# Performance work log

Hardware: AMD Instinct MI355X
Metric: run time of the kernel (lower is better)

Reference implementation:

```python
import jax, jax.numpy as jnp
import numpy as np


def setup_inputs() -> dict:
    key = jax.random.key(0)
    ks = jax.random.split(key, 4)
    B, S, D, U = 4, 4096, 128, 64
    x = jax.random.normal(ks[0], (B, S, D), dtype=jnp.float32)
    Wq = jax.random.normal(ks[1], (D, U), dtype=jnp.float32) * (1.0 / np.sqrt(D))
    Wk = jax.random.normal(ks[2], (D, U), dtype=jnp.float32) * (1.0 / np.sqrt(D))
    Wv = jax.random.normal(ks[3], (D, U), dtype=jnp.float32) * (1.0 / np.sqrt(D))
    bq = jnp.zeros((U,), dtype=jnp.float32)
    bk = jnp.zeros((U,), dtype=jnp.float32)
    bv = jnp.zeros((U,), dtype=jnp.float32)
    return {"x": x, "Wq": Wq, "bq": bq, "Wk": Wk, "bk": bk, "Wv": Wv, "bv": bv}


def reference(x, Wq, bq, Wk, bk, Wv, bv):
    # Single-head, unscaled, unmasked attention (faithful to the Keras layer).
    q = jnp.einsum("bsd,du->bsu", x, Wq) + bq  # [B,S,U]
    k = jnp.einsum("bsd,du->bsu", x, Wk) + bk  # [B,S,U]
    v = jnp.einsum("bsd,du->bsu", x, Wv) + bv  # [B,S,U]
    scores = jnp.einsum("bsu,btu->bst", q, k)  # [B,S,S], no 1/sqrt(d) scaling
    attn = jax.nn.softmax(scores, axis=-1)
    return jnp.einsum("bst,btu->bsu", attn, v)  # [B,S,U]
```

## Files before the change

### kernel.cpp

```cpp
#include <hip/hip_runtime.h>
#include <hip/hip_fp16.h>
#include <math.h>

#define SEQ   4096
#define DIM   128
#define UDIM  64
#define BATCH 4
#define BS    (BATCH*SEQ)
#define NT    (SEQ/64)
#define NSPLIT 6

typedef _Float16 h8 __attribute__((ext_vector_type(8)));
typedef _Float16 h4 __attribute__((ext_vector_type(4)));
typedef _Float16 h2 __attribute__((ext_vector_type(2)));
typedef float    f4 __attribute__((ext_vector_type(4)));

#define MFMA_K32(a,b,c) __builtin_amdgcn_mfma_f32_16x16x32_f16((a),(b),(c),0,0,0)

__device__ __forceinline__ h2 pk2(float a, float b) {
  return __builtin_bit_cast(h2, __builtin_amdgcn_cvt_pkrtz(a, b));
}
__device__ __forceinline__ float fexp2(float x) {
#if __has_builtin(__builtin_amdgcn_exp2f)
  return __builtin_amdgcn_exp2f(x);
#else
  return exp2f(x);
#endif
}

#define WT_STRIDE 272
#define KB_STRIDE 144
#define L2E 1.44269504088896f


__global__ __launch_bounds__(256, 2) void proj_mfma(
    const float* __restrict__ x,
    const float* __restrict__ Wq, const float* __restrict__ bq,
    const float* __restrict__ Wk, const float* __restrict__ bk,
    const float* __restrict__ Wv, const float* __restrict__ bv,
    _Float16* __restrict__ qf, _Float16* __restrict__ kswz, _Float16* __restrict__ vswz)
{
  const int tid  = threadIdx.x;
  const int lane = tid & 63, wv = tid >> 6;
  const int n = lane & 15, quad = lane >> 4;
  const int r0 = blockIdx.x * 64;

  __shared__ __align__(16) char wlds[3][UDIM * WT_STRIDE];
  __shared__ __align__(16) char kbnc[4 * 16 * KB_STRIDE];

  #pragma unroll
  for (int p = 0; p < 3; ++p) {
    const float* __restrict__ W = (p == 0) ? Wq : ((p == 1) ? Wk : Wv);
    #pragma unroll
    for (int i = 0; i < 8; ++i) {
      const int idx = i*256 + tid;
      const int nn  = idx & 63;
      const int k4  = (idx >> 6) * 4;
      const float w0 = W[(k4+0)*UDIM + nn];
      const float w1 = W[(k4+1)*UDIM + nn];
      const float w2 = W[(k4+2)*UDIM + nn];
      const float w3 = W[(k4+3)*UDIM + nn];
      int2 wd;
      wd.x = __builtin_bit_cast(int, pk2(w0, w1));
      wd.y = __builtin_bit_cast(int, pk2(w2, w3));
      *(int2*)(wlds[p] + nn*WT_STRIDE + k4*2) = wd;
    }
  }

  const int row = r0 + wv*16 + n;
  h8 xa[4];
  #pragma unroll
  for (int ks = 0; ks < 4; ++ks) {
    const float* xp = x + (size_t)row*DIM + ks*32 + quad*8;
    const f4 a = *(const f4*)xp, b = *(const f4*)(xp + 4);
    int4 pkd;
    pkd.x = __builtin_bit_cast(int, pk2(a[0], a[1]));
    pkd.y = __builtin_bit_cast(int, pk2(a[2], a[3]));
    pkd.z = __builtin_bit_cast(int, pk2(b[0], b[1]));
    pkd.w = __builtin_bit_cast(int, pk2(b[2], b[3]));
    xa[ks] = __builtin_bit_cast(h8, pkd);
  }
  __syncthreads();

  const int b  = r0 / SEQ;
  const int kb = ((r0 % SEQ) >> 4) + wv;
  const int vt = (r0 % SEQ) >> 6;

  #pragma unroll
  for (int p = 0; p < 3; ++p) {
    const float* __restrict__ bias = (p == 0) ? bq : ((p == 1) ? bk : bv);
    f4 acc[4];
    #pragma unroll
    for (int nt = 0; nt < 4; ++nt) acc[nt] = (f4){0.f,0.f,0.f,0.f};
    #pragma unroll
    for (int ks = 0; ks < 4; ++ks)
      #pragma unroll
      for (int nt = 0; nt < 4; ++nt) {
        const h8 wf = *(const h8*)(wlds[p] + (nt*16 + n)*WT_STRIDE + (ks*32 + quad*8)*2);
        acc[nt] = MFMA_K32(xa[ks], wf, acc[nt]);
      }
    #pragma unroll
    for (int nt = 0; nt < 4; ++nt) {
      const float bb = bias[nt*16 + n];
      #pragma unroll
      for (int r = 0; r < 4; ++r) acc[nt][r] += bb;
    }

    if (p == 0) {
      #pragma unroll
      for (int nt = 0; nt < 4; ++nt)
        #pragma unroll
        for (int r = 0; r < 4; ++r) acc[nt][r] *= L2E;
      const int par = lane & 1;
      const unsigned sel = par ? 0x03020706u : 0x05040100u;
      #pragma unroll
      for (int nt = 0; nt < 4; ++nt)
        #pragma unroll
        for (int pp = 0; pp < 2; ++pp) {
          const int r = 2*pp;
          unsigned A  = __builtin_bit_cast(unsigned, pk2(acc[nt][r], acc[nt][r+1]));
          unsigned Bs = (unsigned)__builtin_amdgcn_mov_dpp((int)A, 0xB1, 0xF, 0xF, true);
          unsigned w  = __builtin_amdgcn_perm(Bs, A, sel);
          const int orow = r0 + wv*16 + 4*quad + r + par;
          const int ocol = nt*16 + n - par;
          *(unsigned*)((char*)qf + ((size_t)orow*UDIM + ocol)*2) = w;
        }
    } else if (p == 1) {
      char* base = kbnc + wv*(16*KB_STRIDE);
      #pragma unroll
      for (int nt = 0; nt < 4; ++nt)
        #pragma unroll
        for (int r = 0; r < 4; ++r)
          *(_Float16*)(base + (4*quad + r)*KB_STRIDE + (nt*16 + n)*2) =
              (_Float16)acc[nt][r];
      _Float16* kdst = kswz + (size_t)b*SEQ*UDIM;
      #pragma unroll
      for (int ks = 0; ks < 2; ++ks) {
        const h8 f = *(const h8*)(base + n*KB_STRIDE + ks*64 + quad*16);
        *(h8*)(kdst + ((size_t)(kb*2 + ks)*64 + lane)*8) = f;
      }
    } else {
      _Float16* vdst = vswz + (size_t)b*SEQ*UDIM + (size_t)vt*4096;
      const int hh = wv >> 1;
      const int qp = 2*(wv & 1) + (quad >> 1);
      const int jb = (quad & 1) * 4;
      #pragma unroll
      for (int nt = 0; nt < 4; ++nt) {
        int2 t;
        t.x = __builtin_bit_cast(int, pk2(acc[nt][0], acc[nt][1]));
        t.y = __builtin_bit_cast(int, pk2(acc[nt][2], acc[nt][3]));
        *(int2*)(vdst + (hh*4 + nt)*512 + (16*qp + n)*8 + jb) = t;
      }
    }
  }
}

__global__ __launch_bounds__(256, 3) void flash_attn_t(
    const _Float16* __restrict__ qf, const _Float16* __restrict__ kswz,
    const _Float16* __restrict__ vswz,
    _Float16* __restrict__ opart, float* __restrict__ Mp, float* __restrict__ Lp)
{
  const int qt = blockIdx.x, b = blockIdx.y, sp = blockIdx.z;
  const int ns = gridDim.z;
  const int kt0 = (sp * NT) / ns;
  const int kt1 = ((sp + 1) * NT) / ns;
  const int tid = threadIdx.x;
  const int lane = tid & 63, wid = tid >> 6;
  const int n = lane & 15, quad = lane >> 4;
  const int qbase = qt*128 + wid*32;

  const _Float16* __restrict__ qb = qf + (size_t)b*SEQ*UDIM;
  const _Float16* kpl = kswz + (size_t)b*SEQ*UDIM + (size_t)kt0*4096 + lane*8;
  const _Float16* kph = kpl + 2048;
  const _Float16* vpl = vswz + (size_t)b*SEQ*UDIM + (size_t)kt0*4096 + lane*8;
  const _Float16* vph = vpl + 2048;

  h8 qB[2][2];
  #pragma unroll
  for (int nt = 0; nt < 2; ++nt)
    #pragma unroll
    for (int ks = 0; ks < 2; ++ks)
      qB[nt][ks] = *(const h8*)(qb + (size_t)(qbase + nt*16 + n)*UDIM + ks*32 + quad*8);

  f4 O[4][2], Ol[2];
  #pragma unroll
  for (int ut = 0; ut < 4; ++ut)
    #pragma unroll
    for (int nt = 0; nt < 2; ++nt) O[ut][nt] = (f4){0.f,0.f,0.f,0.f};
  Ol[0] = (f4){0.f,0.f,0.f,0.f};
  Ol[1] = (f4){0.f,0.f,0.f,0.f};

  float M[2] = {-1e30f, -1e30f};

  h8 ones8;
  { const _Float16 o = (_Float16)1.0f;
    #pragma unroll
    for (int i = 0; i < 8; ++i) ones8[i] = o; }

  const int alo4 = ((32*((lane >> 4) & 1) + (lane & 15)) << 2);
  const int ahi4 = alo4 + 64;
  const bool qlo = (lane < 32);

  h8 ka[4][2];
  ka[0][0] = *(const h8*)(kpl);        ka[0][1] = *(const h8*)(kpl +  512);
  ka[1][0] = *(const h8*)(kpl + 1024); ka[1][1] = *(const h8*)(kpl + 1536);
  ka[2][0] = *(const h8*)(kph);        ka[2][1] = *(const h8*)(kph +  512);
  ka[3][0] = *(const h8*)(kph + 1024); ka[3][1] = *(const h8*)(kph + 1536);

  for (int t = kt0; t < kt1; ++t) {
    h8 va0[4];
    va0[0] = *(const h8*)(vpl);        va0[1] = *(const h8*)(vpl +  512);
    va0[2] = *(const h8*)(vpl + 1024); va0[3] = *(const h8*)(vpl + 1536);

    f4 S[4][2];
    #pragma unroll
    for (int mt = 0; mt < 4; ++mt)
      #pragma unroll
      for (int nt = 0; nt < 2; ++nt) S[mt][nt] = (f4){0.f,0.f,0.f,0.f};
    #pragma unroll
    for (int ks = 0; ks < 2; ++ks)
      #pragma unroll
      for (int mt = 0; mt < 4; ++mt)
        #pragma unroll
        for (int nt = 0; nt < 2; ++nt)
          S[mt][nt] = MFMA_K32(ka[mt][ks], qB[nt][ks], S[mt][nt]);

    if (t + 1 < kt1) {
      kpl += 4096; kph += 4096;
      ka[0][0] = *(const h8*)(kpl);        ka[0][1] = *(const h8*)(kpl +  512);
      ka[1][0] = *(const h8*)(kpl + 1024); ka[1][1] = *(const h8*)(kpl + 1536);
      ka[2][0] = *(const h8*)(kph);        ka[2][1] = *(const h8*)(kph +  512);
      ka[3][0] = *(const h8*)(kph + 1024); ka[3][1] = *(const h8*)(kph + 1536);
    }

    float mn[2];
    #pragma unroll
    for (int nt = 0; nt < 2; ++nt) {
      float m0 = fmaxf(fmaxf(S[0][nt][0], S[0][nt][1]), fmaxf(S[0][nt][2], S[0][nt][3]));
      float m1 = fmaxf(fmaxf(S[1][nt][0], S[1][nt][1]), fmaxf(S[1][nt][2], S[1][nt][3]));
      float m2 = fmaxf(fmaxf(S[2][nt][0], S[2][nt][1]), fmaxf(S[2][nt][2], S[2][nt][3]));
      float m3 = fmaxf(fmaxf(S[3][nt][0], S[3][nt][1]), fmaxf(S[3][nt][2], S[3][nt][3]));
      float rm = fmaxf(fmaxf(m0, m1), fmaxf(m2, m3));
      rm = fmaxf(rm, __shfl_xor(rm, 16));
      rm = fmaxf(rm, __shfl_xor(rm, 32));
      mn[nt] = fmaxf(M[nt], rm);
    }

    const bool nochange = (mn[0] == M[0]) && (mn[1] == M[1]);
    if (!__all(nochange)) {
      #pragma unroll
      for (int nt = 0; nt < 2; ++nt) {
        const float alpha = fexp2(M[nt] - mn[nt]);
        #pragma unroll
        for (int ut = 0; ut < 4; ++ut)
          #pragma unroll
          for (int r = 0; r < 4; ++r) O[ut][nt][r] *= alpha;
        #pragma unroll
        for (int r = 0; r < 4; ++r) Ol[nt][r] *= alpha;
      }
    }
    M[0] = mn[0]; M[1] = mn[1];

    h4 pB[4][2];
    #pragma unroll
    for (int mt = 0; mt < 4; ++mt)
      #pragma unroll
      for (int nt = 0; nt < 2; ++nt) {
        #pragma unroll
        for (int r = 0; r < 4; ++r)
          S[mt][nt][r] = fexp2(S[mt][nt][r] - mn[nt]);
        int2 tt;
        tt.x = __builtin_bit_cast(int, pk2(S[mt][nt][0], S[mt][nt][1]));
        tt.y = __builtin_bit_cast(int, pk2(S[mt][nt][2], S[mt][nt][3]));
        pB[mt][nt] = __builtin_bit_cast(h4, tt);
      }

    h8 pb32a[2];
    #pragma unroll
    for (int nt = 0; nt < 2; ++nt) {
      const int2 X = __builtin_bit_cast(int2, pB[0][nt]);
      const int2 Y = __builtin_bit_cast(int2, pB[1][nt]);
      int4 o;
      { int a0 = __builtin_amdgcn_ds_bpermute(alo4, X.x);
        int b0 = __builtin_amdgcn_ds_bpermute(alo4, Y.x);
        int a1 = __builtin_amdgcn_ds_bpermute(alo4, X.y);
        int b1 = __builtin_amdgcn_ds_bpermute(alo4, Y.y);
        int a2 = __builtin_amdgcn_ds_bpermute(ahi4, X.x);
        int b2 = __builtin_amdgcn_ds_bpermute(ahi4, Y.x);
        int a3 = __builtin_amdgcn_ds_bpermute(ahi4, X.y);
        int b3 = __builtin_amdgcn_ds_bpermute(ahi4, Y.y);
        o.x = qlo ? a0 : b0; o.y = qlo ? a1 : b1;
        o.z = qlo ? a2 : b2; o.w = qlo ? a3 : b3; }
      pb32a[nt] = __builtin_bit_cast(h8, o);
    }

    h8 va1[4];
    va1[0] = *(const h8*)(vph);        va1[1] = *(const h8*)(vph +  512);
    va1[2] = *(const h8*)(vph + 1024); va1[3] = *(const h8*)(vph + 1536);

    #pragma unroll
    for (int ut = 0; ut < 4; ++ut)
      #pragma unroll
      for (int nt = 0; nt < 2; ++nt)
        O[ut][nt] = MFMA_K32(va0[ut], pb32a[nt], O[ut][nt]);
    #pragma unroll
    for (int nt = 0; nt < 2; ++nt)
      Ol[nt] = MFMA_K32(ones8, pb32a[nt], Ol[nt]);

    h8 pb32b[2];
    #pragma unroll
    for (int nt = 0; nt < 2; ++nt) {
      const int2 X = __builtin_bit_cast(int2, pB[2][nt]);
      const int2 Y = __builtin_bit_cast(int2, pB[3][nt]);
      int4 o;
      { int a0 = __builtin_amdgcn_ds_bpermute(alo4, X.x);
        int b0 = __builtin_amdgcn_ds_bpermute(alo4, Y.x);
        int a1 = __builtin_amdgcn_ds_bpermute(alo4, X.y);
        int b1 = __builtin_amdgcn_ds_bpermute(alo4, Y.y);
        int a2 = __builtin_amdgcn_ds_bpermute(ahi4, X.x);
        int b2 = __builtin_amdgcn_ds_bpermute(ahi4, Y.x);
        int a3 = __builtin_amdgcn_ds_bpermute(ahi4, X.y);
        int b3 = __builtin_amdgcn_ds_bpermute(ahi4, Y.y);
        o.x = qlo ? a0 : b0; o.y = qlo ? a1 : b1;
        o.z = qlo ? a2 : b2; o.w = qlo ? a3 : b3; }
      pb32b[nt] = __builtin_bit_cast(h8, o);
    }

    #pragma unroll
    for (int ut = 0; ut < 4; ++ut)
      #pragma unroll
      for (int nt = 0; nt < 2; ++nt)
        O[ut][nt] = MFMA_K32(va1[ut], pb32b[nt], O[ut][nt]);
    #pragma unroll
    for (int nt = 0; nt < 2; ++nt)
      Ol[nt] = MFMA_K32(ones8, pb32b[nt], Ol[nt]);

    vpl += 4096; vph += 4096;
  }

  const size_t rowg = (size_t)sp*BS + (size_t)b*SEQ + qbase;
  #pragma unroll
  for (int nt = 0; nt < 2; ++nt) {
    char* __restrict__ orow = (char*)(opart + (rowg + nt*16 + n)*UDIM);
    #pragma unroll
    for (int ut = 0; ut < 4; ++ut)
      #pragma unroll
      for (int p = 0; p < 2; ++p)
        *(unsigned*)(orow + (ut*16 + quad*4 + 2*p)*2) =
            __builtin_bit_cast(unsigned, pk2(O[ut][nt][2*p], O[ut][nt][2*p+1]));
    if (quad == 0) {
      Mp[rowg + nt*16 + n] = M[nt];
      Lp[rowg + nt*16 + n] = Ol[nt][0];
    }
  }
}

__global__ __launch_bounds__(256) void merge_out(
    const _Float16* __restrict__ opart, const float* __restrict__ Mp,
    const float* __restrict__ Lp, float* __restrict__ out, int nsplit)
{
  const int tid = threadIdx.x;
  const int row = blockIdx.x*16 + (tid >> 4);
  const int u4  = (tid & 15) * 4;
  float M = -1e30f;
  for (int s = 0; s < nsplit; ++s) M = fmaxf(M, Mp[(size_t)s*BS + row]);
  f4 num = (f4){0.f,0.f,0.f,0.f};
  float den = 0.f;
  for (int s = 0; s < nsplit; ++s) {
    const float w = fexp2(Mp[(size_t)s*BS + row] - M);
    den += w * Lp[(size_t)s*BS + row];
    const h4 op = *(const h4*)(opart + ((size_t)s*BS + row)*UDIM + u4);
    #pragma unroll
    for (int i = 0; i < 4; ++i) num[i] += w * (float)op[i];
  }
  const float dinv = 1.f / den;
  *(f4*)(out + (size_t)row*UDIM + u4) = num * dinv;
}

extern "C" void kernel_launch(void* const* d_in, const int* in_sizes, int n_in,
                              void* d_out, int out_size, void* d_ws, size_t ws_size,
                              hipStream_t stream) {
  (void)in_sizes; (void)n_in; (void)out_size;
  const float* x  = (const float*)d_in[0];
  const float* Wq = (const float*)d_in[1];
  const float* bq = (const float*)d_in[2];
  const float* Wk = (const float*)d_in[3];
  const float* bk = (const float*)d_in[4];
  const float* Wv = (const float*)d_in[5];
  const float* bv = (const float*)d_in[6];
  float* out = (float*)d_out;

  char* ws = (char*)d_ws;
  const size_t fBytes = (size_t)BS * UDIM * 2;
  auto need = [](int nsp) {
    return (size_t)3*BS*UDIM*2 + (size_t)nsp*BS*4*2 + (size_t)nsp*BS*UDIM*2;
  };
  int nsplit;
  if      (ws_size >= need(NSPLIT)) nsplit = NSPLIT;
  else if (ws_size >= need(4))      nsplit = 4;
  else if (ws_size >= need(2))      nsplit = 2;
  else                              nsplit = 1;

  _Float16* qf   = (_Float16*)(ws);
  _Float16* kswz = (_Float16*)(ws + fBytes);
  _Float16* vswz = (_Float16*)(ws + 2*fBytes);
  float* Mp      = (float*)(ws + 3*fBytes);
  float* Lp      = (float*)(ws + 3*fBytes + (size_t)nsplit*BS*4);
  _Float16* opart = (_Float16*)(ws + 3*fBytes + (size_t)nsplit*BS*8);

  proj_mfma<<<dim3(BS/64), 256, 0, stream>>>(x, Wq, bq, Wk, bk, Wv, bv, qf, kswz, vswz);
  flash_attn_t<<<dim3(SEQ/128, BATCH, nsplit), 256, 0, stream>>>(
      qf, kswz, vswz, opart, Mp, Lp);
  merge_out<<<dim3(BS/16), 256, 0, stream>>>(opart, Mp, Lp, out, nsplit);
}
```

Measured before the change: 109.6 us.

## Fuse split-KV merge into attention kernel via last-block atomic counter

Drops the separate merge kernel. Each attention block increments a per-(batch, q-tile) atomic counter, and the last split to finish combines all partial outputs into the final result. The counters are zeroed inside the projection kernel. The change also raises wave priority around the MFMA sections with s_setprio. It saves one kernel launch and its tail, at the cost of threadfences, an atomic, and a serial merge tail running in the last block of each tile.

Result: slower. 232.8 us (+112.4%).

```diff
diff --git a/kernel.cpp b/kernel.cpp
--- a/kernel.cpp
+++ b/kernel.cpp
@@ -38,12 +38,15 @@
     const float* __restrict__ Wq, const float* __restrict__ bq,
     const float* __restrict__ Wk, const float* __restrict__ bk,
     const float* __restrict__ Wv, const float* __restrict__ bv,
-    _Float16* __restrict__ qf, _Float16* __restrict__ kswz, _Float16* __restrict__ vswz)
+    _Float16* __restrict__ qf, _Float16* __restrict__ kswz,
+    _Float16* __restrict__ vswz, int* __restrict__ cnt)
 {
   const int tid  = threadIdx.x;
   const int lane = tid & 63, wv = tid >> 6;
   const int n = lane & 15, quad = lane >> 4;
   const int r0 = blockIdx.x * 64;
+
+  if (blockIdx.x < 128 && tid == 0) cnt[blockIdx.x] = 0;
 
   __shared__ __align__(16) char wlds[3][UDIM * WT_STRIDE];
   __shared__ __align__(16) char kbnc[4 * 16 * KB_STRIDE];
@@ -158,7 +161,8 @@
 __global__ __launch_bounds__(256, 3) void flash_attn_t(
     const _Float16* __restrict__ qf, const _Float16* __restrict__ kswz,
     const _Float16* __restrict__ vswz,
-    _Float16* __restrict__ opart, float* __restrict__ Mp, float* __restrict__ Lp)
+    _Float16* __restrict__ opart, float* __restrict__ Mp, float* __restrict__ Lp,
+    int* __restrict__ cnt, float* __restrict__ out)
 {
   const int qt = blockIdx.x, b = blockIdx.y, sp = blockIdx.z;
   const int ns = gridDim.z;
@@ -169,6 +173,8 @@
   const int n = lane & 15, quad = lane >> 4;
   const int qbase = qt*128 + wid*32;
 
+  __shared__ int lastflag;
+
   const _Float16* __restrict__ qb = qf + (size_t)b*SEQ*UDIM;
   const _Float16* kpl = kswz + (size_t)b*SEQ*UDIM + (size_t)kt0*4096 + lane*8;
   const _Float16* kph = kpl + 2048;
@@ -217,6 +223,7 @@
     for (int mt = 0; mt < 4; ++mt)
       #pragma unroll
       for (int nt = 0; nt < 2; ++nt) S[mt][nt] = (f4){0.f,0.f,0.f,0.f};
+    __builtin_amdgcn_s_setprio(1);
     #pragma unroll
     for (int ks = 0; ks < 2; ++ks)
       #pragma unroll
@@ -224,6 +231,7 @@
         #pragma unroll
         for (int nt = 0; nt < 2; ++nt)
           S[mt][nt] = MFMA_K32(ka[mt][ks], qB[nt][ks], S[mt][nt]);
+    __builtin_amdgcn_s_setprio(0);
 
     if (t + 1 < kt1) {
       kpl += 4096; kph += 4096;
@@ -298,6 +306,7 @@
     va1[0] = *(const h8*)(vph);        va1[1] = *(const h8*)(vph +  512);
     va1[2] = *(const h8*)(vph + 1024); va1[3] = *(const h8*)(vph + 1536);
 
+    __builtin_amdgcn_s_setprio(1);
     #pragma unroll
     for (int ut = 0; ut < 4; ++ut)
       #pragma unroll
@@ -306,6 +315,7 @@
     #pragma unroll
     for (int nt = 0; nt < 2; ++nt)
       Ol[nt] = MFMA_K32(ones8, pb32a[nt], Ol[nt]);
+    __builtin_amdgcn_s_setprio(0);
 
     h8 pb32b[2];
     #pragma unroll
@@ -326,6 +336,7 @@
       pb32b[nt] = __builtin_bit_cast(h8, o);
     }
 
+    __builtin_amdgcn_s_setprio(1);
     #pragma unroll
     for (int ut = 0; ut < 4; ++ut)
       #pragma unroll
@@ -334,6 +345,7 @@
     #pragma unroll
     for (int nt = 0; nt < 2; ++nt)
       Ol[nt] = MFMA_K32(ones8, pb32b[nt], Ol[nt]);
+    __builtin_amdgcn_s_setprio(0);
 
     vpl += 4096; vph += 4096;
   }
@@ -353,28 +365,36 @@
       Lp[rowg + nt*16 + n] = Ol[nt][0];
     }
   }
-}
-
-__global__ __launch_bounds__(256) void merge_out(
-    const _Float16* __restrict__ opart, const float* __restrict__ Mp,
-    const float* __restrict__ Lp, float* __restrict__ out, int nsplit)
-{
-  const int tid = threadIdx.x;
-  const int row = blockIdx.x*16 + (tid >> 4);
-  const int u4  = (tid & 15) * 4;
-  float M = -1e30f;
-  for (int s = 0; s < nsplit; ++s) M = fmaxf(M, Mp[(size_t)s*BS + row]);
-  f4 num = (f4){0.f,0.f,0.f,0.f};
-  float den = 0.f;
-  for (int s = 0; s < nsplit; ++s) {
-    const float w = fexp2(Mp[(size_t)s*BS + row] - M);
-    den += w * Lp[(size_t)s*BS + row];
-    const h4 op = *(const h4*)(opart + ((size_t)s*BS + row)*UDIM + u4);
-    #pragma unroll
-    for (int i = 0; i < 4; ++i) num[i] += w * (float)op[i];
-  }
-  const float dinv = 1.f / den;
-  *(f4*)(out + (size_t)row*UDIM + u4) = num * dinv;
+
+  __threadfence();
+  if (tid == 0) {
+    const int old = atomicAdd(&cnt[b*32 + qt], 1);
+    lastflag = (old == ns - 1);
+  }
+  __syncthreads();
+  if (!lastflag) return;
+  __threadfence();
+
+  #pragma unroll
+  for (int it = 0; it < 8; ++it) {
+    const int task = it*256 + tid;
+    const int r    = task >> 4;
+    const int u4   = (task & 15) * 4;
+    const size_t row = (size_t)b*SEQ + qt*128 + r;
+    float Mm = -1e30f;
+    for (int s = 0; s < ns; ++s) Mm = fmaxf(Mm, Mp[(size_t)s*BS + row]);
+    f4 num = (f4){0.f,0.f,0.f,0.f};
+    float den = 0.f;
+    for (int s = 0; s < ns; ++s) {
+      const float w = fexp2(Mp[(size_t)s*BS + row] - Mm);
+      den += w * Lp[(size_t)s*BS + row];
+      const h4 op = *(const h4*)(opart + ((size_t)s*BS + row)*UDIM + u4);
+      #pragma unroll
+      for (int i = 0; i < 4; ++i) num[i] += w * (float)op[i];
+    }
+    const float dinv = 1.f / den;
+    *(f4*)(out + row*UDIM + u4) = num * dinv;
+  }
 }
 
 extern "C" void kernel_launch(void* const* d_in, const int* in_sizes, int n_in,
@@ -393,7 +413,7 @@
   char* ws = (char*)d_ws;
   const size_t fBytes = (size_t)BS * UDIM * 2;
   auto need = [](int nsp) {
-    return (size_t)3*BS*UDIM*2 + (size_t)nsp*BS*4*2 + (size_t)nsp*BS*UDIM*2;
+    return (size_t)3*BS*UDIM*2 + (size_t)nsp*BS*4*2 + (size_t)nsp*BS*UDIM*2 + 512;
   };
   int nsplit;
   if      (ws_size >= need(NSPLIT)) nsplit = NSPLIT;
@@ -401,15 +421,16 @@
   else if (ws_size >= need(2))      nsplit = 2;
   else                              nsplit = 1;
 
-  _Float16* qf   = (_Float16*)(ws);
-  _Float16* kswz = (_Float16*)(ws + fBytes);
-  _Float16* vswz = (_Float16*)(ws + 2*fBytes);
-  float* Mp      = (float*)(ws + 3*fBytes);
-  float* Lp      = (float*)(ws + 3*fBytes + (size_t)nsplit*BS*4);
+  _Float16* qf    = (_Float16*)(ws);
+  _Float16* kswz  = (_Float16*)(ws + fBytes);
+  _Float16* vswz  = (_Float16*)(ws + 2*fBytes);
+  float*    Mp    = (float*)(ws + 3*fBytes);
+  float*    Lp    = (float*)(ws + 3*fBytes + (size_t)nsplit*BS*4);
   _Float16* opart = (_Float16*)(ws + 3*fBytes + (size_t)nsplit*BS*8);
-
-  proj_mfma<<<dim3(BS/64), 256, 0, stream>>>(x, Wq, bq, Wk, bk, Wv, bv, qf, kswz, vswz);
+  int*      cnt   = (int*)(ws + 3*fBytes + (size_t)nsplit*BS*8 + (size_t)nsplit*BS*UDIM*2);
+
+  proj_mfma<<<dim3(BS/64), 256, 0, stream>>>(x, Wq, bq, Wk, bk, Wv, bv,
+                                             qf, kswz, vswz, cnt);
   flash_attn_t<<<dim3(SEQ/128, BATCH, nsplit), 256, 0, stream>>>(
-      qf, kswz, vswz, opart, Mp, Lp);
-  merge_out<<<dim3(BS/16), 256, 0, stream>>>(opart, Mp, Lp, out, nsplit);
+      qf, kswz, vswz, opart, Mp, Lp, cnt, out);
 }
```
